# Kernel optimization log

Hardware: AMD Instinct MI355X
Metric: run time of the kernel (lower is better)

## Reference

```python
import jax, jax.numpy as jnp
import numpy as np

B, G, D = 256, 14, 2048          # batch, grid, vis_embed_dim
H, A, SI, WI, ST = 1024, 512, 1024, 1024, 256  # sent_hidden, att, sent_input, word_input, int_stop
T = 10                           # max_no_of_sent


def _lin(key, out_d, in_d):
    k1, k2 = jax.random.split(key)
    return (jax.random.normal(k1, (out_d, in_d), jnp.float32) * 0.02,
            jax.random.normal(k2, (out_d,), jnp.float32) * 0.02)


def setup_inputs() -> dict:
    key = jax.random.key(0)
    ks = jax.random.split(key, 14)
    inp = {}
    inp['vis_enc_output'] = jax.random.normal(ks[0], (B, G, G, D), jnp.float32)
    inp['captions'] = jax.random.randint(ks[1], (B, T, 20), 0, 1000, jnp.int64 if jax.config.jax_enable_x64 else jnp.int32)
    inp['enc_att_w'], inp['enc_att_b'] = _lin(ks[2], A, D)
    inp['dec_att_w'], inp['dec_att_b'] = _lin(ks[3], A, H)
    inp['full_att_w'], inp['full_att_b'] = _lin(ks[4], 1, A)
    inp['ctx_w'], inp['ctx_b'] = _lin(ks[5], SI, D)
    inp['w_ih'], inp['b_ih'] = _lin(ks[6], 4 * H, SI)
    inp['w_hh'], inp['b_hh'] = _lin(ks[7], 4 * H, H)
    inp['topic_h_w'], inp['topic_h_b'] = _lin(ks[8], WI, H)
    inp['topic_c_w'], inp['topic_c_b'] = _lin(ks[9], WI, SI)
    inp['stop_p_w'], inp['stop_p_b'] = _lin(ks[10], ST, H)
    inp['stop_c_w'], inp['stop_c_b'] = _lin(ks[11], ST, H)
    inp['final_w'], inp['final_b'] = _lin(ks[12], 2, ST)
    return inp


def _forward(vis_enc_output, captions, enc_att_w, enc_att_b, dec_att_w, dec_att_b,
             full_att_w, full_att_b, ctx_w, ctx_b, w_ih, b_ih, w_hh, b_hh,
             topic_h_w, topic_h_b, topic_c_w, topic_c_b,
             stop_p_w, stop_p_b, stop_c_w, stop_c_b, final_w, final_b):
    bsz = vis_enc_output.shape[0]
    v = vis_enc_output.reshape(bsz, -1, vis_enc_output.shape[-1])  # [B, N, D]
    n_sent = captions.shape[1]
    # encoder projection is hoisted out of the loop (same math each step)
    enc_proj = jnp.einsum('bnd,ad->bna', v, enc_att_w) + enc_att_b  # [B, N, A]
    hdim = w_hh.shape[1]

    def step(carry, _):
        h, c = carry
        dec = h @ dec_att_w.T + dec_att_b                            # [B, A]
        join = jnp.tanh(enc_proj + dec[:, None, :])                  # [B, N, A]
        logits = join @ full_att_w[0] + full_att_b[0]                # [B, N]
        scores = jax.nn.softmax(logits, axis=1)
        att_out = jnp.einsum('bn,bnd->bd', scores, v)                # [B, D]
        ctx = att_out @ ctx_w.T + ctx_b                              # [B, SI]
        h_prev = h
        gates = ctx @ w_ih.T + b_ih + h @ w_hh.T + b_hh              # [B, 4H]
        i, f, g, o = jnp.split(gates, 4, axis=1)
        c_new = jax.nn.sigmoid(f) * c + jax.nn.sigmoid(i) * jnp.tanh(g)
        h_new = jax.nn.sigmoid(o) * jnp.tanh(c_new)
        topic = jnp.tanh(h_new @ topic_h_w.T + topic_h_b + ctx @ topic_c_w.T + topic_c_b)
        p = jnp.tanh(h_prev @ stop_p_w.T + stop_p_b + h_new @ stop_c_w.T + stop_c_b)
        p = p @ final_w.T + final_b                                  # [B, 2]
        return (h_new, c_new), (topic, p)

    h0 = jnp.zeros((bsz, hdim), v.dtype)
    c0 = jnp.zeros((bsz, hdim), v.dtype)
    (_, _), (topics, ps) = jax.lax.scan(step, (h0, c0), None, length=n_sent)
    return topics.transpose(1, 0, 2), ps.transpose(1, 0, 2)  # [B, T, WI], [B, T, 2]


def reference(vis_enc_output, captions, enc_att_w, enc_att_b, dec_att_w, dec_att_b,
              full_att_w, full_att_b, ctx_w, ctx_b, w_ih, b_ih, w_hh, b_hh,
              topic_h_w, topic_h_b, topic_c_w, topic_c_b,
              stop_p_w, stop_p_b, stop_c_w, stop_c_b, final_w, final_b):
    return _forward(vis_enc_output, captions, enc_att_w, enc_att_b, dec_att_w, dec_att_b,
                    full_att_w, full_att_b, ctx_w, ctx_b, w_ih, b_ih, w_hh, b_hh,
                    topic_h_w, topic_h_b, topic_c_w, topic_c_b,
                    stop_p_w, stop_p_b, stop_c_w, stop_c_b, final_w, final_b)
```

## Files before the change

### kernel.cpp

```cpp
#include <hip/hip_runtime.h>
#include <cstdint>

#define B_   256
#define NPOS 196
#define D_   2048
#define H_   1024
#define A_   512
#define T_   10

#define N13  6144
#define OFF_DEC    0
#define OFF_WHH    512
#define OFF_STOPP  4608
#define OFF_TOPICH 4864
#define OFF_STOPC  5888
#define NC   5120

#define QMAX 6.5f
#define QSINV (127.f / QMAX)
#define QS    (QMAX / 127.f)

#define PS13 ((size_t)B_ * N13)
#define PSNC ((size_t)B_ * NC)

typedef __attribute__((ext_vector_type(8))) short bf16x8;
typedef __attribute__((ext_vector_type(4))) short bf16x4;
typedef __attribute__((ext_vector_type(4))) float f32x4;

__device__ __forceinline__ float b2f(short s) {
  union { unsigned int u; float f; } c;
  c.u = ((unsigned int)(unsigned short)s) << 16;
  return c.f;
}
__device__ __forceinline__ short f2b(float f) {
  union { float f; unsigned int u; } c; c.f = f;
  unsigned int u = c.u + 0x7fffu + ((c.u >> 16) & 1u);
  return (short)(u >> 16);
}
__device__ __forceinline__ float fast_tanh(float x) {
  float a = fabsf(x);
  float e = __expf(-2.f * a);
  float t = __fdividef(1.f - e, 1.f + e);
  return x < 0.f ? -t : t;
}
__device__ __forceinline__ float fast_sigm(float x) {
  return __fdividef(1.f, 1.f + __expf(-x));
}

#define GLDS16(g, l) __builtin_amdgcn_global_load_lds( \
    (const __attribute__((address_space(1))) void*)(g), \
    (__attribute__((address_space(3))) void*)(l), 16, 0, 0)

__global__ __launch_bounds__(256) void cvtq_v_k(
    const float* __restrict__ in, short* __restrict__ v16,
    unsigned char* __restrict__ v8, long n)
{
  long i = ((long)blockIdx.x * blockDim.x + threadIdx.x) * 8;
  const long stride = (long)gridDim.x * blockDim.x * 8;
  for (; i < n; i += stride) {
    float4 a = *(const float4*)(in + i);
    float4 b = *(const float4*)(in + i + 4);
    bf16x8 o;
    o[0]=f2b(a.x); o[1]=f2b(a.y); o[2]=f2b(a.z); o[3]=f2b(a.w);
    o[4]=f2b(b.x); o[5]=f2b(b.y); o[6]=f2b(b.z); o[7]=f2b(b.w);
    *(bf16x8*)(v16 + i) = o;
    float v[8] = {a.x,a.y,a.z,a.w,b.x,b.y,b.z,b.w};
    unsigned int w0 = 0, w1 = 0;
    #pragma unroll
    for (int j = 0; j < 4; ++j) {
      float q = fminf(fmaxf(rintf(v[j] * QSINV), -127.f), 127.f) + 128.f;
      w0 |= ((unsigned int)(int)q) << (8 * j);
    }
    #pragma unroll
    for (int j = 0; j < 4; ++j) {
      float q = fminf(fmaxf(rintf(v[4+j] * QSINV), -127.f), 127.f) + 128.f;
      w1 |= ((unsigned int)(int)q) << (8 * j);
    }
    uint2 pk; pk.x = w0; pk.y = w1;
    *(uint2*)(v8 + i) = pk;
  }
}

__global__ void cvt_k(const float* __restrict__ in, short* __restrict__ out, long n)
{
  long i = ((long)blockIdx.x * blockDim.x + threadIdx.x) * 8;
  const long stride = (long)gridDim.x * blockDim.x * 8;
  for (; i < n; i += stride) {
    float4 a = *(const float4*)(in + i);
    float4 b = *(const float4*)(in + i + 4);
    bf16x8 o;
    o[0]=f2b(a.x); o[1]=f2b(a.y); o[2]=f2b(a.z); o[3]=f2b(a.w);
    o[4]=f2b(b.x); o[5]=f2b(b.y); o[6]=f2b(b.z); o[7]=f2b(b.w);
    *(bf16x8*)(out + i) = o;
  }
}

struct SegTab {
  const float* src[8];
  short* dst[8];
  int cum[9];
};
__global__ __launch_bounds__(256) void cvt_multi_k(SegTab t)
{
  int seg = 0;
  #pragma unroll
  for (int s = 0; s < 7; ++s) seg += (int)(blockIdx.x >= (unsigned)t.cum[s + 1]);
  const long i = ((long)(blockIdx.x - t.cum[seg]) * 256 + threadIdx.x) * 8;
  const float* in = t.src[seg];
  float4 a = *(const float4*)(in + i);
  float4 b = *(const float4*)(in + i + 4);
  bf16x8 o;
  o[0]=f2b(a.x); o[1]=f2b(a.y); o[2]=f2b(a.z); o[3]=f2b(a.w);
  o[4]=f2b(b.x); o[5]=f2b(b.y); o[6]=f2b(b.z); o[7]=f2b(b.w);
  *(bf16x8*)(t.dst[seg] + i) = o;
}

__global__ __launch_bounds__(256) void transpose_cvt_k(
    const float* __restrict__ in, short* __restrict__ out, int R, int C)
{
  __shared__ float t[32][33];
  const int r0 = blockIdx.y * 32, c0 = blockIdx.x * 32;
  const int tx = threadIdx.x & 31, ty = threadIdx.x >> 5;
  #pragma unroll
  for (int i = 0; i < 32; i += 8)
    t[ty + i][tx] = in[(size_t)(r0 + ty + i) * C + c0 + tx];
  __syncthreads();
  #pragma unroll
  for (int i = 0; i < 32; i += 8)
    out[(size_t)(c0 + ty + i) * R + r0 + tx] = f2b(t[tx][ty + i]);
}

__global__ __launch_bounds__(256) void biasc_k(
    const float* __restrict__ w_ih, const float* __restrict__ b_ih,
    const float* __restrict__ topic_c_w, const float* __restrict__ topic_c_b,
    const float* __restrict__ ctx_b, float* __restrict__ out)
{
  const int r = blockIdx.x * 4 + (threadIdx.x >> 6);
  const int l = threadIdx.x & 63;
  const float* wr; float bb;
  if (r < 4096) { wr = w_ih + (size_t)r * 1024;               bb = b_ih[r]; }
  else          { wr = topic_c_w + (size_t)(r - 4096) * 1024; bb = topic_c_b[r - 4096]; }
  float s = 0.f;
  #pragma unroll
  for (int k = 0; k < 16; ++k) s += wr[l + 64 * k] * ctx_b[l + 64 * k];
  #pragma unroll
  for (int o = 32; o; o >>= 1) s += __shfl_down(s, o);
  if (!l) out[r] = s + bb;
}

__global__ __launch_bounds__(256) void bias13_k(
    const float* __restrict__ dec_att_b, const float* __restrict__ b_hh,
    const float* __restrict__ stop_p_b, const float* __restrict__ topic_h_b,
    const float* __restrict__ stop_c_b, float* __restrict__ bias13)
{
  const int j = blockIdx.x * 256 + threadIdx.x;
  float v;
  if      (j < OFF_WHH)    v = dec_att_b[j];
  else if (j < OFF_STOPP)  v = b_hh[j - OFF_WHH];
  else if (j < OFF_TOPICH) v = stop_p_b[j - OFF_STOPP];
  else if (j < OFF_STOPC)  v = topic_h_b[j - OFF_TOPICH];
  else                     v = stop_c_b[j - OFF_STOPC];
  bias13[j] = v;
}

template<int OUTBF16, int BN, int SWZ, int KZ>
__global__ __launch_bounds__(256) void gemm_bt_k(
    const short* __restrict__ Aptr, const short* __restrict__ Bptr,
    const float* __restrict__ bias, void* __restrict__ Cout,
    int M, int N, int K)
{
  constexpr int TOT = 16 + BN / 8;
  constexpr int NW  = BN / 32;
  __shared__ short As[128 * 64];
  __shared__ short Bs[BN * 64];
  const int tid = threadIdx.x;
  const int l = tid & 63, wv = tid >> 6;
  const int wr = wv >> 1, wc = wv & 1;
  size_t m0, n0;
  if (SWZ) {
    const int id  = blockIdx.y * 4 + blockIdx.x;
    const int xcd = id & 7, s = id >> 3;
    m0 = (size_t)(xcd * 49 + (s >> 2)) * 128;
    n0 = (size_t)(s & 3) * BN;
  } else {
    m0 = (size_t)blockIdx.y * 128;
    n0 = (size_t)blockIdx.x * BN;
  }
  const int srow = l >> 3, scol = (l & 7) * 8;
  const int lr = l & 15, lg = l >> 4;
  const int KC = K / KZ;
  const int kbase = (KZ > 1) ? blockIdx.z * KC : 0;
  const int kend  = kbase + KC;

  f32x4 acc[4][NW];
  #pragma unroll
  for (int i = 0; i < 4; ++i)
    #pragma unroll
    for (int j = 0; j < NW; ++j) acc[i][j] = (f32x4){0.f, 0.f, 0.f, 0.f};

  for (int k0 = kbase; k0 < kend; k0 += 64) {
    #pragma unroll
    for (int i = 0; i < TOT / 4; ++i) {
      const int c = i * 4 + wv;
      if (c < 16) {
        const int row = c * 8 + srow;
        GLDS16(Aptr + (m0 + row) * (size_t)K + k0 + scol, As + c * 512);
      } else {
        const int row = (c - 16) * 8 + srow;
        GLDS16(Bptr + (n0 + row) * (size_t)K + k0 + scol, Bs + (c - 16) * 512);
      }
    }
    __syncthreads();
    #pragma unroll
    for (int kk = 0; kk < 64; kk += 32) {
      bf16x8 af[4], bfr[NW];
      #pragma unroll
      for (int m = 0; m < 4; ++m)
        af[m] = *(const bf16x8*)(As + (wr * 64 + m * 16 + lr) * 64 + kk + lg * 8);
      #pragma unroll
      for (int n = 0; n < NW; ++n)
        bfr[n] = *(const bf16x8*)(Bs + (wc * (BN / 2) + n * 16 + lr) * 64 + kk + lg * 8);
      #pragma unroll
      for (int m = 0; m < 4; ++m)
        #pragma unroll
        for (int n = 0; n < NW; ++n)
          acc[m][n] = __builtin_amdgcn_mfma_f32_16x16x32_bf16(af[m], bfr[n], acc[m][n], 0, 0, 0);
    }
    __syncthreads();
  }

  #pragma unroll
  for (int m = 0; m < 4; ++m) {
    const size_t row = m0 + wr * 64 + m * 16 + lg * 4;
    #pragma unroll
    for (int n = 0; n < NW; ++n) {
      const size_t col = n0 + wc * (BN / 2) + n * 16 + lr;
      if (KZ > 1) {
        float* Cp = (float*)Cout + (size_t)blockIdx.z * M * (size_t)N;
        #pragma unroll
        for (int r = 0; r < 4; ++r)
          Cp[(row + r) * (size_t)N + col] = acc[m][n][r];
      } else {
        const float bv = bias[col];
        #pragma unroll
        for (int r = 0; r < 4; ++r) {
          const float v = acc[m][n][r] + bv;
          if (OUTBF16) ((short*)Cout)[(row + r) * (size_t)N + col] = f2b(v);
          else         ((float*)Cout)[(row + r) * (size_t)N + col] = v;
        }
      }
    }
  }
}

template<int DO_FINAL, int DO_SCORES>
__global__ __launch_bounds__(512) void scores_k(
    const float* __restrict__ pcur, const float* __restrict__ pprev,
    const float* __restrict__ g3p, const float* __restrict__ biasc,
    const float* __restrict__ bias13,
    const short* __restrict__ encp, const float* __restrict__ fullw,
    const float* __restrict__ finw, const float* __restrict__ finb,
    float* __restrict__ scbuf, float* __restrict__ out_t,
    float* __restrict__ out_p, int tprev)
{
  const int j = blockIdx.x, b = blockIdx.y, tid = threadIdx.x;
  const int l = tid & 63, wv = tid >> 6;
  const size_t b13 = (size_t)b * N13;
  __shared__ float dec_s[A_], fw_s[A_], pp[256];

  if (DO_FINAL) {
    float* ot = out_t + (size_t)b * (T_ * 1024) + (size_t)tprev * 1024;
    const int jj = j * 512 + tid;
    float th = bias13[OFF_TOPICH + jj] + pcur[b13 + OFF_TOPICH + jj]
             + pcur[PS13 + b13 + OFF_TOPICH + jj];
    float tc = biasc[4096 + jj];
    #pragma unroll
    for (int z = 0; z < 4; ++z) tc += g3p[z * PSNC + (size_t)b * NC + 4096 + jj];
    ot[jj] = fast_tanh(th + tc);
    if (j == 0 && tid < 256) {
      float a = bias13[OFF_STOPP + tid] + pprev[b13 + OFF_STOPP + tid]
              + pprev[PS13 + b13 + OFF_STOPP + tid];
      float c = bias13[OFF_STOPC + tid] + pcur[b13 + OFF_STOPC + tid]
              + pcur[PS13 + b13 + OFF_STOPC + tid];
      pp[tid] = fast_tanh(a + c);
    }
  }
  if (DO_SCORES) {
    dec_s[tid] = pcur[b13 + tid] + pcur[PS13 + b13 + tid] + bias13[tid];
    fw_s[tid]  = fullw[tid];
  }
  __syncthreads();

  if (DO_FINAL && j == 0 && wv < 2) {
    float s = 0.f;
    #pragma unroll
    for (int k = 0; k < 4; ++k) s += pp[l + 64 * k] * finw[wv * 256 + l + 64 * k];
    #pragma unroll
    for (int o = 32; o; o >>= 1) s += __shfl_down(s, o);
    if (!l) out_p[(size_t)b * (T_ * 2) + tprev * 2 + wv] = s + finb[wv];
  }

  if (DO_SCORES) {
    const short* ep = encp + ((size_t)b * NPOS + j * 98) * A_;
    for (int n = wv; n < 98; n += 8) {
      bf16x8 e = *(const bf16x8*)(ep + (size_t)n * A_ + l * 8);
      float s = 0.f;
      #pragma unroll
      for (int k = 0; k < 8; ++k)
        s += fast_tanh(b2f(e[k]) + dec_s[l * 8 + k]) * fw_s[l * 8 + k];
      #pragma unroll
      for (int o = 32; o; o >>= 1) s += __shfl_down(s, o);
      if (!l) scbuf[(size_t)b * NPOS + j * 98 + n] = s;
    }
  }
}

template<int VMODE>
__global__ __launch_bounds__(256) void pv_k(
    const void* __restrict__ vptr, const float* __restrict__ scbuf,
    short* __restrict__ attout)
{
  const int b = blockIdx.y;
  const int dbase = blockIdx.x * 512;
  const int tid = threadIdx.x;
  const int l = tid & 63, grp = tid >> 6;
  __shared__ float sc[NPOS];
  __shared__ float red[8];
  __shared__ float tmp[3][512];

  const float lg = (tid < NPOS) ? scbuf[(size_t)b * NPOS + tid] : -3e38f;
  float lm = lg;
  #pragma unroll
  for (int o = 32; o; o >>= 1) lm = fmaxf(lm, __shfl_down(lm, o));
  if (!l) red[grp] = lm;
  __syncthreads();
  const float mx = fmaxf(fmaxf(red[0], red[1]), fmaxf(red[2], red[3]));
  const float ev = (tid < NPOS) ? __expf(lg - mx) : 0.f;
  float es = ev;
  #pragma unroll
  for (int o = 32; o; o >>= 1) es += __shfl_down(es, o);
  if (!l) red[4 + grp] = es;
  __syncthreads();
  const float inv = __fdividef(1.f, red[4] + red[5] + red[6] + red[7]);
  if (tid < NPOS) sc[tid] = ev * inv;
  __syncthreads();

  const int dt = l * 8;
  float a[8] = {0,0,0,0,0,0,0,0};
  if (VMODE == 1) {
    const unsigned char* vb = (const unsigned char*)vptr
        + (size_t)b * NPOS * D_ + dbase + dt;
    #pragma unroll 7
    for (int n = grp; n < NPOS; n += 4) {
      const float s = sc[n];
      const uint2 w = *(const uint2*)(vb + (size_t)n * D_);
      a[0] += s * (float)(w.x & 255u);
      a[1] += s * (float)((w.x >> 8) & 255u);
      a[2] += s * (float)((w.x >> 16) & 255u);
      a[3] += s * (float)(w.x >> 24);
      a[4] += s * (float)(w.y & 255u);
      a[5] += s * (float)((w.y >> 8) & 255u);
      a[6] += s * (float)((w.y >> 16) & 255u);
      a[7] += s * (float)(w.y >> 24);
    }
  } else {
    const float* vf = (const float*)vptr + (size_t)b * NPOS * D_ + dbase + dt;
    #pragma unroll 2
    for (int n = grp; n < NPOS; n += 4) {
      const float s = sc[n];
      float4 v0 = *(const float4*)(vf + (size_t)n * D_);
      float4 v1 = *(const float4*)(vf + (size_t)n * D_ + 4);
      a[0] += s*v0.x; a[1] += s*v0.y; a[2] += s*v0.z; a[3] += s*v0.w;
      a[4] += s*v1.x; a[5] += s*v1.y; a[6] += s*v1.z; a[7] += s*v1.w;
    }
  }
  if (grp) {
    #pragma unroll
    for (int k = 0; k < 8; ++k) tmp[grp - 1][dt + k] = a[k];
  }
  __syncthreads();
  if (!grp) {
    bf16x8 o8;
    #pragma unroll
    for (int k = 0; k < 8; ++k) {
      float v = a[k] + tmp[0][dt + k] + tmp[1][dt + k] + tmp[2][dt + k];
      if (VMODE == 1) v = v * QS - 128.f * QS;
      o8[k] = f2b(v);
    }
    *(bf16x8*)(attout + (size_t)b * D_ + dbase + dt) = o8;
  }
}

__global__ __launch_bounds__(128) void lstm_k(
    const float* __restrict__ g3p, const float* __restrict__ gPp,
    const float* __restrict__ biasc, const float* __restrict__ bias13,
    float* __restrict__ c, short* __restrict__ hbf)
{
  const int idx = (blockIdx.x * 128 + threadIdx.x) * 4;
  const int b = idx >> 10, j = idx & 1023;
  f32x4 gate[4];
  #pragma unroll
  for (int g = 0; g < 4; ++g) {
    const size_t base  = (size_t)b * NC + g * 1024 + j;
    const size_t baseh = (size_t)b * N13 + OFF_WHH + g * 1024 + j;
    f32x4 s = *(const f32x4*)(biasc + g * 1024 + j);
    s += *(const f32x4*)(bias13 + OFF_WHH + g * 1024 + j);
    #pragma unroll
    for (int z = 0; z < 4; ++z) s += *(const f32x4*)(g3p + z * PSNC + base);
    #pragma unroll
    for (int z = 0; z < 2; ++z) s += *(const f32x4*)(gPp + z * PS13 + baseh);
    gate[g] = s;
  }
  f32x4 cv = *(const f32x4*)(c + idx);
  f32x4 cn;
  bf16x4 hn;
  #pragma unroll
  for (int k = 0; k < 4; ++k) {
    const float nc2 = fast_sigm(gate[1][k]) * cv[k]
                    + fast_sigm(gate[0][k]) * fast_tanh(gate[2][k]);
    cn[k] = nc2;
    hn[k] = f2b(fast_sigm(gate[3][k]) * fast_tanh(nc2));
  }
  *(f32x4*)(c + idx) = cn;
  *(bf16x4*)(hbf + idx) = hn;
}

extern "C" void kernel_launch(void* const* d_in, const int* in_sizes, int n_in,
                              void* d_out, int out_size, void* d_ws, size_t ws_size,
                              hipStream_t stream)
{
  const float* vis       = (const float*)d_in[0];
  const float* enc_att_w = (const float*)d_in[2];
  const float* enc_att_b = (const float*)d_in[3];
  const float* dec_att_w = (const float*)d_in[4];
  const float* dec_att_b = (const float*)d_in[5];
  const float* full_att_w= (const float*)d_in[6];
  const float* ctx_w     = (const float*)d_in[8];
  const float* ctx_b     = (const float*)d_in[9];
  const float* w_ih      = (const float*)d_in[10];
  const float* b_ih      = (const float*)d_in[11];
  const float* w_hh      = (const float*)d_in[12];
  const float* b_hh      = (const float*)d_in[13];
  const float* topic_h_w = (const float*)d_in[14];
  const float* topic_h_b = (const float*)d_in[15];
  const float* topic_c_w = (const float*)d_in[16];
  const float* topic_c_b = (const float*)d_in[17];
  const float* stop_p_w  = (const float*)d_in[18];
  const float* stop_p_b  = (const float*)d_in[19];
  const float* stop_c_w  = (const float*)d_in[20];
  const float* stop_c_b  = (const float*)d_in[21];
  const float* final_w   = (const float*)d_in[22];
  const float* final_b   = (const float*)d_in[23];

  uint8_t* wsp = (uint8_t*)d_ws;
  size_t off = 0;
  auto take = [&](size_t bytes) -> void* {
    void* p = wsp + off;
    off = (off + bytes + 255) & ~(size_t)255;
    return p;
  };

  short* encproj = (short*)take((size_t)B_ * NPOS * A_ * 2);
  short* encw    = (short*)take((size_t)A_ * D_ * 2);
  short* w2cat   = (short*)take((size_t)NC * 1024 * 2);
  short* ctxwT   = (short*)take((size_t)D_ * 1024 * 2);
  short* Wc      = (short*)take((size_t)NC * D_ * 2);
  short* w13     = (short*)take((size_t)N13 * H_ * 2);
  float* biasc   = (float*)take((size_t)NC * 4);
  float* bias13  = (float*)take((size_t)N13 * 4);
  float* zeros   = (float*)take((size_t)D_ * 4);
  short* hbf     = (short*)take((size_t)B_ * H_ * 2);
  float* cst     = (float*)take((size_t)B_ * H_ * 4);
  float* pairs0  = (float*)take(2 * PS13 * 4);
  float* pairs1  = (float*)take(2 * PS13 * 4);
  float* g3p     = (float*)take(4 * PSNC * 4);
  short* attb    = (short*)take((size_t)B_ * D_ * 2);
  float* scbuf   = (float*)take((size_t)B_ * NPOS * 4);
  const size_t base0 = off;
  const long   nv = (long)B_ * NPOS * D_;
  unsigned char* v8 = (unsigned char*)take((size_t)nv);
  short* v16 = (short*)(wsp + off);
  const bool full = (ws_size >= off + (size_t)nv * 2);

  float* out_t = (float*)d_out;
  float* out_p = (float*)d_out + (size_t)B_ * T_ * 1024;

  {
    SegTab t;
    const float* srcs[8] = {enc_att_w, w_ih, topic_c_w, dec_att_w, w_hh,
                            stop_p_w, topic_h_w, stop_c_w};
    short* dsts[8] = {encw, w2cat, w2cat + (size_t)4096 * 1024,
                      w13 + (size_t)OFF_DEC * 1024, w13 + (size_t)OFF_WHH * 1024,
                      w13 + (size_t)OFF_STOPP * 1024, w13 + (size_t)OFF_TOPICH * 1024,
                      w13 + (size_t)OFF_STOPC * 1024};
    const int nel[8] = {1048576, 4194304, 1048576, 524288, 4194304, 262144, 1048576, 262144};
    int c = 0;
    for (int i = 0; i < 8; ++i) {
      t.src[i] = srcs[i]; t.dst[i] = dsts[i];
      t.cum[i] = c; c += nel[i] / 2048;
    }
    t.cum[8] = c;
    cvt_multi_k<<<c, 256, 0, stream>>>(t);
  }
  transpose_cvt_k<<<dim3(D_ / 32, 1024 / 32), 256, 0, stream>>>(ctx_w, ctxwT, 1024, D_);
  hipMemsetAsync(zeros, 0, (size_t)D_ * 4, stream);
  gemm_bt_k<1, 128, 0, 1><<<dim3(D_ / 128, NC / 128), 256, 0, stream>>>(
      w2cat, ctxwT, zeros, Wc, NC, D_, 1024);
  biasc_k<<<NC / 4, 256, 0, stream>>>(w_ih, b_ih, topic_c_w, topic_c_b, ctx_b, biasc);
  bias13_k<<<N13 / 256, 256, 0, stream>>>(
      dec_att_b, b_hh, stop_p_b, topic_h_b, stop_c_b, bias13);
  hipMemsetAsync(cst, 0, (size_t)B_ * H_ * 4, stream);
  hipMemsetAsync(pairs1, 0, 2 * PS13 * 4, stream);

  const int Mrows = B_ * NPOS;
  if (full) {
    cvtq_v_k<<<8192, 256, 0, stream>>>(vis, v16, v8, nv);
    gemm_bt_k<1, 128, 1, 1><<<dim3(A_ / 128, Mrows / 128), 256, 0, stream>>>(
        v16, encw, enc_att_b, encproj, Mrows, A_, D_);
  } else {
    const size_t avail = (ws_size > base0) ? ws_size - base0 : 0;
    int dt = 1;
    const int cand[] = {56, 28, 14, 8, 7, 4, 2, 1};
    for (int c : cand)
      if ((392 % c) == 0 && (size_t)c * 128 * D_ * 2 <= avail) { dt = c; break; }
    short* vchunk = (short*)(wsp + base0);
    const int CR = dt * 128;
    for (int s = 0; s < Mrows; s += CR) {
      cvt_k<<<4096, 256, 0, stream>>>(vis + (size_t)s * D_, vchunk, (long)CR * D_);
      gemm_bt_k<1, 128, 0, 1><<<dim3(A_ / 128, dt), 256, 0, stream>>>(
          vchunk, encw, enc_att_b, encproj + (size_t)s * A_, CR, A_, D_);
    }
  }

  for (int t = 0; t < T_; ++t) {
    float* pcur  = (t & 1) ? pairs0 : pairs1;
    float* pprev = (t & 1) ? pairs1 : pairs0;
    if (t == 0)
      scores_k<0, 1><<<dim3(2, B_), 512, 0, stream>>>(pcur, pprev, g3p, biasc, bias13,
          encproj, full_att_w, final_w, final_b, scbuf, out_t, out_p, 0);
    else
      scores_k<1, 1><<<dim3(2, B_), 512, 0, stream>>>(pcur, pprev, g3p, biasc, bias13,
          encproj, full_att_w, final_w, final_b, scbuf, out_t, out_p, t - 1);
    if (full) pv_k<1><<<dim3(4, B_), 256, 0, stream>>>(v8, scbuf, attb);
    else      pv_k<0><<<dim3(4, B_), 256, 0, stream>>>(vis, scbuf, attb);
    gemm_bt_k<0, 128, 0, 4><<<dim3(NC / 128, B_ / 128, 4), 256, 0, stream>>>(
        attb, Wc, nullptr, g3p, B_, NC, D_);
    lstm_k<<<(B_ * H_) / 512, 128, 0, stream>>>(g3p, pcur, biasc, bias13, cst, hbf);
    float* pnew = (t & 1) ? pairs1 : pairs0;
    gemm_bt_k<0, 64, 0, 2><<<dim3(N13 / 64, B_ / 128, 2), 256, 0, stream>>>(
        hbf, w13, nullptr, pnew, B_, N13, H_);
  }
  {
    float* pcur  = ((T_ - 1) & 1) ? pairs1 : pairs0;
    float* pprev = ((T_ - 1) & 1) ? pairs0 : pairs1;
    scores_k<1, 0><<<dim3(2, B_), 512, 0, stream>>>(pcur, pprev, g3p, biasc, bias13,
        encproj, full_att_w, final_w, final_b, scbuf, out_t, out_p, T_ - 1);
  }
}
```

Measured before the change: 1.130 ms.

## Fuse fp32-to-bf16 conversion and int8 quantization into encoder projection GEMM

The separate pass that turned the visual features into a bf16 copy and an int8 copy is removed. A new encoder projection GEMM now reads fp32 features directly, packs them to bf16 in LDS with v_cvt_pk_bf16_f32, and emits the int8 quantized copy from the blocks with the first N tile. This avoids writing and re-reading a ~200MB bf16 intermediate. In exchange, A-tile loads now go through registers instead of direct-to-LDS loads, and the fp32 A data is read once for each of the four N tiles.

Measured after the change: 1.471 ms. 1.3x slower.

```diff
diff --git a/kernel.cpp b/kernel.cpp
--- a/kernel.cpp
+++ b/kernel.cpp
@@ -37,6 +37,11 @@
   unsigned int u = c.u + 0x7fffu + ((c.u >> 16) & 1u);
   return (short)(u >> 16);
 }
+__device__ __forceinline__ unsigned int pk_bf16(float lo, float hi) {
+  unsigned int r;
+  asm volatile("v_cvt_pk_bf16_f32 %0, %1, %2" : "=v"(r) : "v"(lo), "v"(hi));
+  return r;
+}
 __device__ __forceinline__ float fast_tanh(float x) {
   float a = fabsf(x);
   float e = __expf(-2.f * a);
@@ -50,50 +55,6 @@
 #define GLDS16(g, l) __builtin_amdgcn_global_load_lds( \
     (const __attribute__((address_space(1))) void*)(g), \
     (__attribute__((address_space(3))) void*)(l), 16, 0, 0)
-
-__global__ __launch_bounds__(256) void cvtq_v_k(
-    const float* __restrict__ in, short* __restrict__ v16,
-    unsigned char* __restrict__ v8, long n)
-{
-  long i = ((long)blockIdx.x * blockDim.x + threadIdx.x) * 8;
-  const long stride = (long)gridDim.x * blockDim.x * 8;
-  for (; i < n; i += stride) {
-    float4 a = *(const float4*)(in + i);
-    float4 b = *(const float4*)(in + i + 4);
-    bf16x8 o;
-    o[0]=f2b(a.x); o[1]=f2b(a.y); o[2]=f2b(a.z); o[3]=f2b(a.w);
-    o[4]=f2b(b.x); o[5]=f2b(b.y); o[6]=f2b(b.z); o[7]=f2b(b.w);
-    *(bf16x8*)(v16 + i) = o;
-    float v[8] = {a.x,a.y,a.z,a.w,b.x,b.y,b.z,b.w};
-    unsigned int w0 = 0, w1 = 0;
-    #pragma unroll
-    for (int j = 0; j < 4; ++j) {
-      float q = fminf(fmaxf(rintf(v[j] * QSINV), -127.f), 127.f) + 128.f;
-      w0 |= ((unsigned int)(int)q) << (8 * j);
-    }
-    #pragma unroll
-    for (int j = 0; j < 4; ++j) {
-      float q = fminf(fmaxf(rintf(v[4+j] * QSINV), -127.f), 127.f) + 128.f;
-      w1 |= ((unsigned int)(int)q) << (8 * j);
-    }
-    uint2 pk; pk.x = w0; pk.y = w1;
-    *(uint2*)(v8 + i) = pk;
-  }
-}
-
-__global__ void cvt_k(const float* __restrict__ in, short* __restrict__ out, long n)
-{
-  long i = ((long)blockIdx.x * blockDim.x + threadIdx.x) * 8;
-  const long stride = (long)gridDim.x * blockDim.x * 8;
-  for (; i < n; i += stride) {
-    float4 a = *(const float4*)(in + i);
-    float4 b = *(const float4*)(in + i + 4);
-    bf16x8 o;
-    o[0]=f2b(a.x); o[1]=f2b(a.y); o[2]=f2b(a.z); o[3]=f2b(a.w);
-    o[4]=f2b(b.x); o[5]=f2b(b.y); o[6]=f2b(b.z); o[7]=f2b(b.w);
-    *(bf16x8*)(out + i) = o;
-  }
-}
 
 struct SegTab {
   const float* src[8];
@@ -163,7 +124,7 @@
   bias13[j] = v;
 }
 
-template<int OUTBF16, int BN, int SWZ, int KZ>
+template<int OUTBF16, int BN, int KZ>
 __global__ __launch_bounds__(256) void gemm_bt_k(
     const short* __restrict__ Aptr, const short* __restrict__ Bptr,
     const float* __restrict__ bias, void* __restrict__ Cout,
@@ -176,16 +137,8 @@
   const int tid = threadIdx.x;
   const int l = tid & 63, wv = tid >> 6;
   const int wr = wv >> 1, wc = wv & 1;
-  size_t m0, n0;
-  if (SWZ) {
-    const int id  = blockIdx.y * 4 + blockIdx.x;
-    const int xcd = id & 7, s = id >> 3;
-    m0 = (size_t)(xcd * 49 + (s >> 2)) * 128;
-    n0 = (size_t)(s & 3) * BN;
-  } else {
-    m0 = (size_t)blockIdx.y * 128;
-    n0 = (size_t)blockIdx.x * BN;
-  }
+  const size_t m0 = (size_t)blockIdx.y * 128;
+  const size_t n0 = (size_t)blockIdx.x * BN;
   const int srow = l >> 3, scol = (l & 7) * 8;
   const int lr = l & 15, lg = l >> 4;
   const int KC = K / KZ;
@@ -249,6 +202,93 @@
           else         ((float*)Cout)[(row + r) * (size_t)N + col] = v;
         }
       }
+    }
+  }
+}
+
+template<int QW>
+__global__ __launch_bounds__(256) void encproj_k(
+    const float* __restrict__ Afp, const short* __restrict__ Bptr,
+    const float* __restrict__ bias, short* __restrict__ Cout,
+    unsigned char* __restrict__ v8)
+{
+  constexpr int K = D_;
+  constexpr int N = A_;
+  __shared__ short As[128 * 64];
+  __shared__ short Bs[128 * 64];
+  const int tid = threadIdx.x;
+  const int l = tid & 63, wv = tid >> 6;
+  const int wr = wv >> 1, wc = wv & 1;
+  const int id  = blockIdx.y * 4 + blockIdx.x;
+  const int xcd = id & 7, s = id >> 3;
+  const size_t m0 = (size_t)(xcd * 49 + (s >> 2)) * 128;
+  const size_t n0 = (size_t)(s & 3) * 128;
+  const bool doq = QW && ((s & 3) == 0);
+  const int srow = l >> 3, scol = (l & 7) * 8;
+  const int arow = tid >> 4;
+  const int acol = (tid & 15) * 4;
+  const int lr = l & 15, lg = l >> 4;
+
+  f32x4 acc[4][4];
+  #pragma unroll
+  for (int i = 0; i < 4; ++i)
+    #pragma unroll
+    for (int j = 0; j < 4; ++j) acc[i][j] = (f32x4){0.f, 0.f, 0.f, 0.f};
+
+  for (int k0 = 0; k0 < K; k0 += 64) {
+    #pragma unroll
+    for (int i = 0; i < 4; ++i) {
+      const int c = i * 4 + wv;
+      GLDS16(Bptr + (n0 + c * 8 + srow) * (size_t)K + k0 + scol, Bs + c * 512);
+    }
+    #pragma unroll
+    for (int p = 0; p < 8; ++p) {
+      const int row = p * 16 + arow;
+      const float4 a = *(const float4*)(Afp + (m0 + row) * (size_t)K + k0 + acol);
+      uint2 w;
+      w.x = pk_bf16(a.x, a.y);
+      w.y = pk_bf16(a.z, a.w);
+      *(uint2*)(As + row * 64 + acol) = w;
+      if (doq) {
+        unsigned int q = 0;
+        const float vv[4] = {a.x, a.y, a.z, a.w};
+        #pragma unroll
+        for (int j = 0; j < 4; ++j) {
+          float t = fminf(fmaxf(rintf(vv[j] * QSINV), -127.f), 127.f) + 128.f;
+          q |= ((unsigned int)(int)t) << (8 * j);
+        }
+        *(unsigned int*)(v8 + (m0 + row) * (size_t)K + k0 + acol) = q;
+      }
+    }
+    __syncthreads();
+    #pragma unroll
+    for (int kk = 0; kk < 64; kk += 32) {
+      bf16x8 af[4], bfr[4];
+      #pragma unroll
+      for (int m = 0; m < 4; ++m)
+        af[m] = *(const bf16x8*)(As + (wr * 64 + m * 16 + lr) * 64 + kk + lg * 8);
+      #pragma unroll
+      for (int n = 0; n < 4; ++n)
+        bfr[n] = *(const bf16x8*)(Bs + (wc * 64 + n * 16 + lr) * 64 + kk + lg * 8);
+      #pragma unroll
+      for (int m = 0; m < 4; ++m)
+        #pragma unroll
+        for (int n = 0; n < 4; ++n)
+          acc[m][n] = __builtin_amdgcn_mfma_f32_16x16x32_bf16(af[m], bfr[n], acc[m][n], 0, 0, 0);
+    }
+    __syncthreads();
+  }
+
+  #pragma unroll
+  for (int m = 0; m < 4; ++m) {
+    const size_t row = m0 + wr * 64 + m * 16 + lg * 4;
+    #pragma unroll
+    for (int n = 0; n < 4; ++n) {
+      const size_t col = n0 + wc * 64 + n * 16 + lr;
+      const float bv = bias[col];
+      #pragma unroll
+      for (int r = 0; r < 4; ++r)
+        Cout[(row + r) * (size_t)N + col] = f2b(acc[m][n][r] + bv);
     }
   }
 }
@@ -476,11 +516,9 @@
   float* g3p     = (float*)take(4 * PSNC * 4);
   short* attb    = (short*)take((size_t)B_ * D_ * 2);
   float* scbuf   = (float*)take((size_t)B_ * NPOS * 4);
-  const size_t base0 = off;
-  const long   nv = (long)B_ * NPOS * D_;
+  const long nv = (long)B_ * NPOS * D_;
   unsigned char* v8 = (unsigned char*)take((size_t)nv);
-  short* v16 = (short*)(wsp + off);
-  const bool full = (ws_size >= off + (size_t)nv * 2);
+  const bool full = (ws_size >= off);
 
   float* out_t = (float*)d_out;
   float* out_p = (float*)d_out + (size_t)B_ * T_ * 1024;
@@ -504,7 +542,7 @@
   }
   transpose_cvt_k<<<dim3(D_ / 32, 1024 / 32), 256, 0, stream>>>(ctx_w, ctxwT, 1024, D_);
   hipMemsetAsync(zeros, 0, (size_t)D_ * 4, stream);
-  gemm_bt_k<1, 128, 0, 1><<<dim3(D_ / 128, NC / 128), 256, 0, stream>>>(
+  gemm_bt_k<1, 128, 1><<<dim3(D_ / 128, NC / 128), 256, 0, stream>>>(
       w2cat, ctxwT, zeros, Wc, NC, D_, 1024);
   biasc_k<<<NC / 4, 256, 0, stream>>>(w_ih, b_ih, topic_c_w, topic_c_b, ctx_b, biasc);
   bias13_k<<<N13 / 256, 256, 0, stream>>>(
@@ -512,25 +550,10 @@
   hipMemsetAsync(cst, 0, (size_t)B_ * H_ * 4, stream);
   hipMemsetAsync(pairs1, 0, 2 * PS13 * 4, stream);
 
-  const int Mrows = B_ * NPOS;
-  if (full) {
-    cvtq_v_k<<<8192, 256, 0, stream>>>(vis, v16, v8, nv);
-    gemm_bt_k<1, 128, 1, 1><<<dim3(A_ / 128, Mrows / 128), 256, 0, stream>>>(
-        v16, encw, enc_att_b, encproj, Mrows, A_, D_);
-  } else {
-    const size_t avail = (ws_size > base0) ? ws_size - base0 : 0;
-    int dt = 1;
-    const int cand[] = {56, 28, 14, 8, 7, 4, 2, 1};
-    for (int c : cand)
-      if ((392 % c) == 0 && (size_t)c * 128 * D_ * 2 <= avail) { dt = c; break; }
-    short* vchunk = (short*)(wsp + base0);
-    const int CR = dt * 128;
-    for (int s = 0; s < Mrows; s += CR) {
-      cvt_k<<<4096, 256, 0, stream>>>(vis + (size_t)s * D_, vchunk, (long)CR * D_);
-      gemm_bt_k<1, 128, 0, 1><<<dim3(A_ / 128, dt), 256, 0, stream>>>(
-          vchunk, encw, enc_att_b, encproj + (size_t)s * A_, CR, A_, D_);
-    }
-  }
+  if (full)
+    encproj_k<1><<<dim3(4, 392), 256, 0, stream>>>(vis, encw, enc_att_b, encproj, v8);
+  else
+    encproj_k<0><<<dim3(4, 392), 256, 0, stream>>>(vis, encw, enc_att_b, encproj, nullptr);
 
   for (int t = 0; t < T_; ++t) {
     float* pcur  = (t & 1) ? pairs0 : pairs1;
@@ -543,11 +566,11 @@
           encproj, full_att_w, final_w, final_b, scbuf, out_t, out_p, t - 1);
     if (full) pv_k<1><<<dim3(4, B_), 256, 0, stream>>>(v8, scbuf, attb);
     else      pv_k<0><<<dim3(4, B_), 256, 0, stream>>>(vis, scbuf, attb);
-    gemm_bt_k<0, 128, 0, 4><<<dim3(NC / 128, B_ / 128, 4), 256, 0, stream>>>(
+    gemm_bt_k<0, 128, 4><<<dim3(NC / 128, B_ / 128, 4), 256, 0, stream>>>(
         attb, Wc, nullptr, g3p, B_, NC, D_);
     lstm_k<<<(B_ * H_) / 512, 128, 0, stream>>>(g3p, pcur, biasc, bias13, cst, hbf);
     float* pnew = (t & 1) ? pairs1 : pairs0;
-    gemm_bt_k<0, 64, 0, 2><<<dim3(N13 / 64, B_ / 128, 2), 256, 0, stream>>>(
+    gemm_bt_k<0, 64, 2><<<dim3(N13 / 64, B_ / 128, 2), 256, 0, stream>>>(
         hbf, w13, nullptr, pnew, B_, N13, H_);
   }
   {
```
